# Kernel tuning notes

Hardware: AMD Instinct MI355X
Metric: run time of the kernel (lower is better)

The kernel has to match this reference:

```python
import jax, jax.numpy as jnp
import numpy as np

B, T, DIN = 1024, 256, 128
UNITS, OUT = 512, 64
INTER, CMD, MOTOR = 269, 179, 64  # AutoNCP(512, 64) layer split
SENS_FANOUT, INTER_FANOUT, MOTOR_FANIN = 134, 89, 89
LAYER_DIMS = [(DIN, INTER), (INTER, CMD), (CMD, MOTOR)]


def _layer_mask(rng, n_in, n_h, fanout=None, fanin=None):
    # sparse prev-layer -> layer block, dense recurrent block (ncps WiredCfCCell)
    m = np.zeros((n_in, n_h), dtype=bool)
    if fanout is not None:
        for i in range(n_in):
            m[i, rng.choice(n_h, size=fanout, replace=False)] = True
    else:
        for j in range(n_h):
            m[rng.choice(n_in, size=fanin, replace=False), j] = True
    full = np.concatenate([m, np.ones((n_h, n_h), dtype=bool)], axis=0)
    return jnp.asarray(full.T)  # (n_h, n_in + n_h): Linear weight layout


def setup_inputs() -> dict:
    key = jax.random.key(0)
    ks = jax.random.split(key, 30)
    rng = np.random.RandomState(22222)
    d = {}
    d["x"] = jax.random.normal(ks[0], (B, T, DIN), dtype=jnp.float32)
    d["hidden"] = jnp.zeros((B, UNITS), dtype=jnp.float32)
    d["mask0"] = _layer_mask(rng, DIN, INTER, fanout=SENS_FANOUT)
    d["mask1"] = _layer_mask(rng, INTER, CMD, fanout=INTER_FANOUT)
    d["mask2"] = _layer_mask(rng, CMD, MOTOR, fanin=MOTOR_FANIN)
    ki = 1
    for li, (n_in, n_h) in enumerate(LAYER_DIMS):
        cat = n_in + n_h
        s = 1.0 / float(np.sqrt(cat))
        for nm in ("ff1", "ff2", "ta", "tb"):
            d[f"{nm}_w{li}"] = jax.random.uniform(ks[ki], (n_h, cat), minval=-s, maxval=s, dtype=jnp.float32); ki += 1
            d[f"{nm}_b{li}"] = jax.random.uniform(ks[ki], (n_h,), minval=-s, maxval=s, dtype=jnp.float32); ki += 1
    sf = 1.0 / float(np.sqrt(MOTOR))
    d["fc_w"] = jax.random.uniform(ks[ki], (OUT, MOTOR), minval=-sf, maxval=sf, dtype=jnp.float32)
    d["fc_b"] = jax.random.uniform(ks[ki + 1], (OUT,), minval=-sf, maxval=sf, dtype=jnp.float32)
    return d


def _cfc_cell(inp, h, w1, b1, w2, b2, wa, ba, wb, bb):
    xc = jnp.concatenate([inp, h], axis=-1)
    ff1 = jnp.tanh(xc @ w1.T + b1)
    ff2 = jnp.tanh(xc @ w2.T + b2)
    ts = 1.0  # default elapsed time in CfC when no timespans given
    t_interp = jax.nn.sigmoid((xc @ wa.T + ba) * ts + (xc @ wb.T + bb))
    return ff1 * (1.0 - t_interp) + t_interp * ff2


def reference(x, hidden, mask0, mask1, mask2,
              ff1_w0, ff1_b0, ff2_w0, ff2_b0, ta_w0, ta_b0, tb_w0, tb_b0,
              ff1_w1, ff1_b1, ff2_w1, ff2_b1, ta_w1, ta_b1, tb_w1, tb_b1,
              ff1_w2, ff1_b2, ff2_w2, ff2_b2, ta_w2, ta_b2, tb_w2, tb_b2,
              fc_w, fc_b):
    m0 = mask0.astype(ff1_w0.dtype)
    m1 = mask1.astype(ff1_w1.dtype)
    m2 = mask2.astype(ff1_w2.dtype)
    layers = (
        (ff1_w0 * m0, ff1_b0, ff2_w0 * m0, ff2_b0, ta_w0, ta_b0, tb_w0, tb_b0),
        (ff1_w1 * m1, ff1_b1, ff2_w1 * m1, ff2_b1, ta_w1, ta_b1, tb_w1, tb_b1),
        (ff1_w2 * m2, ff1_b2, ff2_w2 * m2, ff2_b2, ta_w2, ta_b2, tb_w2, tb_b2),
    )
    h0 = hidden[:, :INTER]
    h1 = hidden[:, INTER:INTER + CMD]
    h2 = hidden[:, INTER + CMD:]

    def step(carry, xt):
        c0, c1, c2 = carry
        n0 = _cfc_cell(xt, c0, *layers[0])  # inter layer
        n1 = _cfc_cell(n0, c1, *layers[1])  # command layer
        n2 = _cfc_cell(n1, c2, *layers[2])  # motor layer
        return (n0, n1, n2), n2

    (f0, f1, f2), outs = jax.lax.scan(step, (h0, h1, h2), jnp.swapaxes(x, 0, 1))
    predictions = jnp.einsum('tbm,om->bto', outs, fc_w) + fc_b  # (B,T,OUT)
    hn = jnp.concatenate([f0, f1, f2], axis=-1)  # (B,UNITS)
    return predictions, hn
```

## Files before the change

kernel.cpp:

```cpp
#include <hip/hip_runtime.h>
#include <math.h>


namespace {
constexpr int kBatch = 1024;
constexpr int kT     = 256;
constexpr int kDIN   = 128;
constexpr int kUNITS = 512;
constexpr int kINTER = 269;
constexpr int kCMD   = 179;
constexpr int kMOTOR = 64;
constexpr int kOUT   = 64;

constexpr int kCAT0 = kDIN + kINTER;
constexpr int kCAT1 = kINTER + kCMD;
constexpr int kCAT2 = kCMD + kMOTOR;

constexpr int kC0r = 3 * kINTER;
constexpr int kC1r = 3 * kCMD;
constexpr int kC2r = 3 * kMOTOR;
constexpr int kC0p = 808;
constexpr int kC1p = 538;
constexpr int kC2p = 192;
constexpr int kP0 = 404;
constexpr int kP1 = 269;
constexpr int kP2 = 96;
constexpr int kK40 = 100;
constexpr int kK41 = 112;
constexpr int kK42 = 64;
constexpr int kS0 = kK40 * 4;
constexpr int kS1 = kK41 * 4;
constexpr int kS2 = kK42 * 4;

constexpr int kQ0 = kK40 * kC0p;
constexpr int kQ1 = kK41 * kC1p;
constexpr int kQ2 = kK42 * kC2p;
constexpr int kQ  = kQ0 + kQ1 + kQ2;
constexpr int kBCN = kC0p + kC1p + kC2p;
constexpr int kBCOff = kQ * 4;

constexpr int kMT = 4;
constexpr int kNT = 1024;

static_assert(kK40 % 4 == 0 && kK41 % 4 == 0 && kK42 % 4 == 0, "ping-pong");
}

__device__ __forceinline__ int detect_mask_mode(const void* m0) {
  const unsigned int* w = (const unsigned int*)m0;
  if (w[32] == 0x01010101u && w[33] == 0x01010101u &&
      w[34] == 0x01010101u && w[35] == 0x01010101u)
    return 0;
  if (w[128] == 0x3F800000u && w[129] == 0x3F800000u && w[130] == 0x3F800000u)
    return 2;
  return 1;
}

__device__ __forceinline__ bool mask_at(const void* mk, int idx, int mode) {
  if (mode == 0) return ((const unsigned char*)mk)[idx] != 0;
  if (mode == 1) return ((const int*)mk)[idx] != 0;
  return ((const float*)mk)[idx] != 0.0f;
}

__global__ void prep_kernel(
    const void* __restrict__ m0_, const void* __restrict__ m1_,
    const void* __restrict__ m2_,
    const float* __restrict__ f1w0, const float* __restrict__ f2w0,
    const float* __restrict__ taw0, const float* __restrict__ tbw0,
    const float* __restrict__ f1w1, const float* __restrict__ f2w1,
    const float* __restrict__ taw1, const float* __restrict__ tbw1,
    const float* __restrict__ f1w2, const float* __restrict__ f2w2,
    const float* __restrict__ taw2, const float* __restrict__ tbw2,
    const float* __restrict__ f1b0, const float* __restrict__ f2b0,
    const float* __restrict__ tab0, const float* __restrict__ tbb0,
    const float* __restrict__ f1b1, const float* __restrict__ f2b1,
    const float* __restrict__ tab1, const float* __restrict__ tbb1,
    const float* __restrict__ f1b2, const float* __restrict__ f2b2,
    const float* __restrict__ tab2, const float* __restrict__ tbb2,
    float* __restrict__ ws) {
  int i = blockIdx.x * 256 + threadIdx.x;
  const int mode = detect_mask_mode(m0_);
  if (i < kQ) {
    int qi, NCp, ncols, cat, nh, baseq;
    const void* mk;
    const float *wf1, *wf2, *wta, *wtb;
    if (i < kQ0) {
      qi = i; NCp = kC0p; ncols = kC0r; cat = kCAT0; nh = kINTER; mk = m0_;
      wf1 = f1w0; wf2 = f2w0; wta = taw0; wtb = tbw0; baseq = 0;
    } else if (i < kQ0 + kQ1) {
      qi = i - kQ0; NCp = kC1p; ncols = kC1r; cat = kCAT1; nh = kCMD; mk = m1_;
      wf1 = f1w1; wf2 = f2w1; wta = taw1; wtb = tbw1; baseq = kQ0;
    } else {
      qi = i - kQ0 - kQ1; NCp = kC2p; ncols = kC2r; cat = kCAT2; nh = kMOTOR;
      mk = m2_;
      wf1 = f1w2; wf2 = f2w2; wta = taw2; wtb = tbw2; baseq = kQ0 + kQ1;
    }
    int k4 = qi / NCp;
    int j  = qi % NCp;
    float v[4] = {0.0f, 0.0f, 0.0f, 0.0f};
    if (j < ncols) {
#pragma unroll
      for (int kk = 0; kk < 4; ++kk) {
        int k = k4 * 4 + kk;
        float r = 0.0f;
        if (k < cat) {
          if (j < nh) {
            r = mask_at(mk, j * cat + k, mode) ? wf1[j * cat + k] : 0.0f;
          } else if (j < 2 * nh) {
            int jj = j - nh;
            r = mask_at(mk, jj * cat + k, mode) ? wf2[jj * cat + k] : 0.0f;
          } else {
            int jj = j - 2 * nh;
            r = wta[jj * cat + k] + wtb[jj * cat + k];
          }
        }
        v[kk] = r;
      }
    }
    ((float4*)ws)[baseq + qi] = make_float4(v[0], v[1], v[2], v[3]);
  } else if (i < kQ + kBCN) {
    int pos = i - kQ;
    int j = pos;
    int nh, ncols;
    const float *bf1, *bf2, *bta, *btb;
    if (j < kC0p) {
      nh = kINTER; ncols = kC0r;
      bf1 = f1b0; bf2 = f2b0; bta = tab0; btb = tbb0;
    } else if (j < kC0p + kC1p) {
      j -= kC0p; nh = kCMD; ncols = kC1r;
      bf1 = f1b1; bf2 = f2b1; bta = tab1; btb = tbb1;
    } else {
      j -= kC0p + kC1p; nh = kMOTOR; ncols = kC2r;
      bf1 = f1b2; bf2 = f2b2; bta = tab2; btb = tbb2;
    }
    float r = 0.0f;
    if (j < ncols) {
      if (j < nh) r = bf1[j];
      else if (j < 2 * nh) r = bf2[j - nh];
      else r = bta[j - 2 * nh] + btb[j - 2 * nh];
    }
    ws[kBCOff + pos] = r;
  }
}

template <int AST>
__device__ __forceinline__ void fma_blk(const float4 wA, const float4 wB,
                                        const float* __restrict__ ak,
                                        float (&aA)[kMT], float (&aB)[kMT]) {
#pragma unroll
  for (int r = 0; r < kMT; ++r) {
    float4 av = *(const float4*)(ak + r * AST);
    aA[r] = fmaf(wA.x, av.x, aA[r]);
    aA[r] = fmaf(wA.y, av.y, aA[r]);
    aA[r] = fmaf(wA.z, av.z, aA[r]);
    aA[r] = fmaf(wA.w, av.w, aA[r]);
    aB[r] = fmaf(wB.x, av.x, aB[r]);
    aB[r] = fmaf(wB.y, av.y, aB[r]);
    aB[r] = fmaf(wB.z, av.z, aB[r]);
    aB[r] = fmaf(wB.w, av.w, aB[r]);
  }
}

template <int NK4, int NCOLS, int AST, int PST>
__device__ __forceinline__ void mv2(const float4* __restrict__ wp,
                                    const float* __restrict__ a,
                                    float* __restrict__ pc,
                                    const float* __restrict__ bias,
                                    int jA, int jB) {
  float aA[kMT], aB[kMT];
  const float bA = bias[jA], bB = bias[jB];
#pragma unroll
  for (int r = 0; r < kMT; ++r) { aA[r] = bA; aB[r] = bB; }
  const float4* pA = wp + jA;
  const float4* pB = wp + jB;
  float4 wA0 = pA[0 * NCOLS], wB0 = pB[0 * NCOLS];
  float4 wA1 = pA[1 * NCOLS], wB1 = pB[1 * NCOLS];
  float4 vA0 = pA[2 * NCOLS], vB0 = pB[2 * NCOLS];
  float4 vA1 = pA[3 * NCOLS], vB1 = pB[3 * NCOLS];
  const float* ak = a;
  int k4 = 0;
#pragma unroll 1
  for (; k4 + 8 <= NK4; k4 += 4) {
    fma_blk<AST>(wA0, wB0, ak, aA, aB);
    fma_blk<AST>(wA1, wB1, ak + 4, aA, aB);
    wA0 = pA[(k4 + 4) * NCOLS]; wB0 = pB[(k4 + 4) * NCOLS];
    wA1 = pA[(k4 + 5) * NCOLS]; wB1 = pB[(k4 + 5) * NCOLS];
    fma_blk<AST>(vA0, vB0, ak + 8, aA, aB);
    fma_blk<AST>(vA1, vB1, ak + 12, aA, aB);
    vA0 = pA[(k4 + 6) * NCOLS]; vB0 = pB[(k4 + 6) * NCOLS];
    vA1 = pA[(k4 + 7) * NCOLS]; vB1 = pB[(k4 + 7) * NCOLS];
    ak += 16;
  }
  fma_blk<AST>(wA0, wB0, ak, aA, aB);
  fma_blk<AST>(wA1, wB1, ak + 4, aA, aB);
  fma_blk<AST>(vA0, vB0, ak + 8, aA, aB);
  fma_blk<AST>(vA1, vB1, ak + 12, aA, aB);
#pragma unroll
  for (int r = 0; r < kMT; ++r) {
    pc[r * PST + jA] = aA[r];
    pc[r * PST + jB] = aB[r];
  }
}

__device__ __forceinline__ float cfc_combine(float p1, float p2, float pt) {
  float f1 = tanhf(p1);
  float f2 = tanhf(p2);
  float ti = 1.0f / (1.0f + expf(-pt));
  return f1 + ti * (f2 - f1);
}

__global__ __launch_bounds__(kNT) void ncp_main(
    const float* __restrict__ x, const float* __restrict__ hidden,
    const float* __restrict__ ws, const float* __restrict__ fcw,
    const float* __restrict__ fcb, float* __restrict__ out) {
  __shared__ __align__(16) float xc0[kMT][kS0];
  __shared__ __align__(16) float xc1[kMT][kS1];
  __shared__ __align__(16) float xc2[kMT][kS2];
  __shared__ __align__(16) float pa0[kMT][kC0p];
  __shared__ __align__(16) float pa1[kMT][kC1p];
  __shared__ __align__(16) float pa2[kMT][kC2p];
  __shared__ float s_fcwT[64 * 64];
  __shared__ float s_bc[kBCN];
  __shared__ float s_fcb[64];

  const int tid = threadIdx.x;
  const int b0 = blockIdx.x * kMT;

#pragma unroll
  for (int r = 0; r < kMT; ++r) {
    if (tid < kS0) xc0[r][tid] = 0.0f;
    if (tid < kS1) xc1[r][tid] = 0.0f;
    if (tid < kS2) xc2[r][tid] = 0.0f;
  }
  __syncthreads();
  for (int i = tid; i < kMT * kUNITS; i += kNT) {
    int r = i >> 9, u = i & 511;
    float v = hidden[(size_t)(b0 + r) * kUNITS + u];
    if (u < kINTER) xc0[r][kDIN + u] = v;
    else if (u < kINTER + kCMD) xc1[r][u] = v;
    else xc2[r][kCMD + (u - (kINTER + kCMD))] = v;
  }
  for (int i = tid; i < kBCN; i += kNT) s_bc[i] = ws[kBCOff + i];
  if (tid < 64) s_fcb[tid] = fcb[tid];
  for (int i = tid; i < 64 * 64; i += kNT) {
    int m = i >> 6, o = i & 63;
    s_fcwT[i] = fcw[o * 64 + m];
  }
  if (tid < 128) {
    int r = tid >> 5, d4 = tid & 31;
    *(float4*)&xc0[r][d4 * 4] =
        *(const float4*)&x[(size_t)(b0 + r) * (kT * kDIN) + d4 * 4];
  }
  __syncthreads();

  const float4* wp0 = (const float4*)ws;
  const float4* wp1 = wp0 + kQ0;
  const float4* wp2 = wp1 + kQ1;

  for (int p = 0; p < kT + 3; ++p) {
    if (tid < 448) {
      if (p < kT && tid < kP0)
        mv2<kK40, kC0p, kS0, kC0p>(wp0, &xc0[0][0], &pa0[0][0], s_bc,
                                   tid, tid + kP0);
    } else if (tid < 768) {
      const int pi = tid - 448;
      if (p >= 1 && p <= kT && pi < kP1)
        mv2<kK41, kC1p, kS1, kC1p>(wp1, &xc1[0][0], &pa1[0][0], s_bc + kC0p,
                                   pi, pi + kP1);
    } else if (tid < 896) {
      const int pi = tid - 768;
      if (p >= 2 && p <= kT + 1 && pi < kP2)
        mv2<kK42, kC2p, kS2, kC2p>(wp2, &xc2[0][0], &pa2[0][0],
                                   s_bc + kC0p + kC1p, pi, pi + kP2);
    } else if (p >= 3) {
      const int i2 = tid - 896;
      const int o = i2 & 63;
      const int rb = (i2 >> 6) << 1;
      const int t_fc = p - 3;
      float a0 = s_fcb[o], a1 = s_fcb[o];
      for (int m = 0; m < kMOTOR; ++m) {
        float w = s_fcwT[m * 64 + o];
        a0 = fmaf(xc2[rb][kCMD + m], w, a0);
        a1 = fmaf(xc2[rb + 1][kCMD + m], w, a1);
      }
      size_t base = (size_t)(b0 + rb) * (kT * kOUT) + (size_t)t_fc * kOUT + o;
      out[base] = a0;
      out[base + (size_t)kT * kOUT] = a1;
    }
    __syncthreads();
    if (tid < kINTER) {
      if (p < kT) {
#pragma unroll
        for (int r = 0; r < kMT; ++r) {
          float v = cfc_combine(pa0[r][tid], pa0[r][tid + kINTER],
                                pa0[r][tid + 2 * kINTER]);
          xc1[r][tid] = v;
          xc0[r][kDIN + tid] = v;
        }
      }
    } else if (tid >= 448 && tid < 448 + kCMD) {
      if (p >= 1 && p <= kT) {
        const int j = tid - 448;
#pragma unroll
        for (int r = 0; r < kMT; ++r) {
          float v = cfc_combine(pa1[r][j], pa1[r][j + kCMD],
                                pa1[r][j + 2 * kCMD]);
          xc2[r][j] = v;
          xc1[r][kINTER + j] = v;
        }
      }
    } else if (tid >= 768 && tid < 768 + kMOTOR) {
      if (p >= 2 && p <= kT + 1) {
        const int j = tid - 768;
#pragma unroll
        for (int r = 0; r < kMT; ++r) {
          float v = cfc_combine(pa2[r][j], pa2[r][j + kMOTOR],
                                pa2[r][j + 2 * kMOTOR]);
          xc2[r][kCMD + j] = v;
        }
      }
    } else if (tid >= 896) {
      if (p + 1 < kT) {
        const int i2 = tid - 896;
        const int r = i2 >> 5, d4 = i2 & 31;
        *(float4*)&xc0[r][d4 * 4] =
            *(const float4*)&x[(size_t)(b0 + r) * (kT * kDIN) +
                               (size_t)(p + 1) * kDIN + d4 * 4];
      }
    }
    __syncthreads();
  }

  const size_t hnoff = (size_t)kBatch * kT * kOUT;
  for (int i = tid; i < kMT * kUNITS; i += kNT) {
    int r = i >> 9, u = i & 511;
    float v;
    if (u < kINTER) v = xc0[r][kDIN + u];
    else if (u < kINTER + kCMD) v = xc1[r][u];
    else v = xc2[r][kCMD + (u - (kINTER + kCMD))];
    out[hnoff + (size_t)(b0 + r) * kUNITS + u] = v;
  }
}

extern "C" void kernel_launch(void* const* d_in, const int* in_sizes, int n_in,
                              void* d_out, int out_size, void* d_ws, size_t ws_size,
                              hipStream_t stream) {
  (void)in_sizes; (void)n_in; (void)out_size; (void)ws_size;
  const float* x = (const float*)d_in[0];
  const float* hidden = (const float*)d_in[1];
  const void* m0 = d_in[2];
  const void* m1 = d_in[3];
  const void* m2 = d_in[4];
  const float* f1w0 = (const float*)d_in[5];
  const float* f1b0 = (const float*)d_in[6];
  const float* f2w0 = (const float*)d_in[7];
  const float* f2b0 = (const float*)d_in[8];
  const float* taw0 = (const float*)d_in[9];
  const float* tab0 = (const float*)d_in[10];
  const float* tbw0 = (const float*)d_in[11];
  const float* tbb0 = (const float*)d_in[12];
  const float* f1w1 = (const float*)d_in[13];
  const float* f1b1 = (const float*)d_in[14];
  const float* f2w1 = (const float*)d_in[15];
  const float* f2b1 = (const float*)d_in[16];
  const float* taw1 = (const float*)d_in[17];
  const float* tab1 = (const float*)d_in[18];
  const float* tbw1 = (const float*)d_in[19];
  const float* tbb1 = (const float*)d_in[20];
  const float* f1w2 = (const float*)d_in[21];
  const float* f1b2 = (const float*)d_in[22];
  const float* f2w2 = (const float*)d_in[23];
  const float* f2b2 = (const float*)d_in[24];
  const float* taw2 = (const float*)d_in[25];
  const float* tab2 = (const float*)d_in[26];
  const float* tbw2 = (const float*)d_in[27];
  const float* tbb2 = (const float*)d_in[28];
  const float* fcw = (const float*)d_in[29];
  const float* fcb = (const float*)d_in[30];
  float* ws = (float*)d_ws;
  float* out = (float*)d_out;

  const int prep_items = kQ + kBCN;
  prep_kernel<<<(prep_items + 255) / 256, 256, 0, stream>>>(
      m0, m1, m2,
      f1w0, f2w0, taw0, tbw0,
      f1w1, f2w1, taw1, tbw1,
      f1w2, f2w2, taw2, tbw2,
      f1b0, f2b0, tab0, tbb0,
      f1b1, f2b1, tab1, tbb1,
      f1b2, f2b2, tab2, tbb2,
      ws);

  ncp_main<<<kBatch / kMT, kNT, 0, stream>>>(x, hidden, ws, fcw, fcb, out);
}
```

Measured before the change: 8.694 ms.

## Compute four adjacent output columns per thread and shrink block to 768 threads

Each matvec thread now computes four adjacent output columns instead of two strided ones. Each shared-memory activation read feeds four columns, and results go out as float4 stores. The block drops from 1024 to 768 threads, with the role ranges (layer matvecs, combine, x prefetch, FC output) remapped. The FC output stage now uses 64 threads that each handle four rows. The goal is less LDS traffic per FMA and less per-step barrier cost. The cost is more registers per thread (16 accumulators plus 16 float4 weight registers) and fewer threads to hide latency.

```diff
diff --git a/kernel.cpp b/kernel.cpp
--- a/kernel.cpp
+++ b/kernel.cpp
@@ -20,11 +20,11 @@
 constexpr int kC1r = 3 * kCMD;
 constexpr int kC2r = 3 * kMOTOR;
 constexpr int kC0p = 808;
-constexpr int kC1p = 538;
+constexpr int kC1p = 540;
 constexpr int kC2p = 192;
-constexpr int kP0 = 404;
-constexpr int kP1 = 269;
-constexpr int kP2 = 96;
+constexpr int kP0 = 202;
+constexpr int kP1 = 135;
+constexpr int kP2 = 48;
 constexpr int kK40 = 100;
 constexpr int kK41 = 112;
 constexpr int kK42 = 64;
@@ -40,9 +40,10 @@
 constexpr int kBCOff = kQ * 4;
 
 constexpr int kMT = 4;
-constexpr int kNT = 1024;
+constexpr int kNT = 768;
 
 static_assert(kK40 % 4 == 0 && kK41 % 4 == 0 && kK42 % 4 == 0, "ping-pong");
+static_assert(kC0p % 4 == 0 && kC1p % 4 == 0 && kC2p % 4 == 0, "4-col");
 }
 
 __device__ __forceinline__ int detect_mask_mode(const void* m0) {
@@ -143,61 +144,71 @@
 }
 
 template <int AST>
-__device__ __forceinline__ void fma_blk(const float4 wA, const float4 wB,
-                                        const float* __restrict__ ak,
-                                        float (&aA)[kMT], float (&aB)[kMT]) {
+__device__ __forceinline__ void fma4(const float4 (&w)[4],
+                                     const float* __restrict__ ak,
+                                     float (&acc)[4][kMT]) {
 #pragma unroll
   for (int r = 0; r < kMT; ++r) {
     float4 av = *(const float4*)(ak + r * AST);
-    aA[r] = fmaf(wA.x, av.x, aA[r]);
-    aA[r] = fmaf(wA.y, av.y, aA[r]);
-    aA[r] = fmaf(wA.z, av.z, aA[r]);
-    aA[r] = fmaf(wA.w, av.w, aA[r]);
-    aB[r] = fmaf(wB.x, av.x, aB[r]);
-    aB[r] = fmaf(wB.y, av.y, aB[r]);
-    aB[r] = fmaf(wB.z, av.z, aB[r]);
-    aB[r] = fmaf(wB.w, av.w, aB[r]);
+#pragma unroll
+    for (int c = 0; c < 4; ++c) {
+      acc[c][r] = fmaf(w[c].x, av.x, acc[c][r]);
+      acc[c][r] = fmaf(w[c].y, av.y, acc[c][r]);
+      acc[c][r] = fmaf(w[c].z, av.z, acc[c][r]);
+      acc[c][r] = fmaf(w[c].w, av.w, acc[c][r]);
+    }
   }
 }
 
 template <int NK4, int NCOLS, int AST, int PST>
-__device__ __forceinline__ void mv2(const float4* __restrict__ wp,
+__device__ __forceinline__ void mv4(const float4* __restrict__ wp,
                                     const float* __restrict__ a,
                                     float* __restrict__ pc,
                                     const float* __restrict__ bias,
-                                    int jA, int jB) {
-  float aA[kMT], aB[kMT];
-  const float bA = bias[jA], bB = bias[jB];
-#pragma unroll
-  for (int r = 0; r < kMT; ++r) { aA[r] = bA; aB[r] = bB; }
-  const float4* pA = wp + jA;
-  const float4* pB = wp + jB;
-  float4 wA0 = pA[0 * NCOLS], wB0 = pB[0 * NCOLS];
-  float4 wA1 = pA[1 * NCOLS], wB1 = pB[1 * NCOLS];
-  float4 vA0 = pA[2 * NCOLS], vB0 = pB[2 * NCOLS];
-  float4 vA1 = pA[3 * NCOLS], vB1 = pB[3 * NCOLS];
+                                    int jq) {
+  const float4* pw = wp + 4 * jq;
+  float acc[4][kMT];
+#pragma unroll
+  for (int c = 0; c < 4; ++c) {
+    const float b = bias[4 * jq + c];
+#pragma unroll
+    for (int r = 0; r < kMT; ++r) acc[c][r] = b;
+  }
+  float4 U0[4], U1[4], V0[4], V1[4];
+#pragma unroll
+  for (int c = 0; c < 4; ++c) {
+    U0[c] = pw[0 * NCOLS + c];
+    U1[c] = pw[1 * NCOLS + c];
+    V0[c] = pw[2 * NCOLS + c];
+    V1[c] = pw[3 * NCOLS + c];
+  }
   const float* ak = a;
-  int k4 = 0;
 #pragma unroll 1
-  for (; k4 + 8 <= NK4; k4 += 4) {
-    fma_blk<AST>(wA0, wB0, ak, aA, aB);
-    fma_blk<AST>(wA1, wB1, ak + 4, aA, aB);
-    wA0 = pA[(k4 + 4) * NCOLS]; wB0 = pB[(k4 + 4) * NCOLS];
-    wA1 = pA[(k4 + 5) * NCOLS]; wB1 = pB[(k4 + 5) * NCOLS];
-    fma_blk<AST>(vA0, vB0, ak + 8, aA, aB);
-    fma_blk<AST>(vA1, vB1, ak + 12, aA, aB);
-    vA0 = pA[(k4 + 6) * NCOLS]; vB0 = pB[(k4 + 6) * NCOLS];
-    vA1 = pA[(k4 + 7) * NCOLS]; vB1 = pB[(k4 + 7) * NCOLS];
+  for (int k4 = 0; k4 + 8 <= NK4; k4 += 4) {
+    fma4<AST>(U0, ak, acc);
+    fma4<AST>(U1, ak + 4, acc);
+#pragma unroll
+    for (int c = 0; c < 4; ++c) {
+      U0[c] = pw[(k4 + 4) * NCOLS + c];
+      U1[c] = pw[(k4 + 5) * NCOLS + c];
+    }
+    fma4<AST>(V0, ak + 8, acc);
+    fma4<AST>(V1, ak + 12, acc);
+#pragma unroll
+    for (int c = 0; c < 4; ++c) {
+      V0[c] = pw[(k4 + 6) * NCOLS + c];
+      V1[c] = pw[(k4 + 7) * NCOLS + c];
+    }
     ak += 16;
   }
-  fma_blk<AST>(wA0, wB0, ak, aA, aB);
-  fma_blk<AST>(wA1, wB1, ak + 4, aA, aB);
-  fma_blk<AST>(vA0, vB0, ak + 8, aA, aB);
-  fma_blk<AST>(vA1, vB1, ak + 12, aA, aB);
+  fma4<AST>(U0, ak, acc);
+  fma4<AST>(U1, ak + 4, acc);
+  fma4<AST>(V0, ak + 8, acc);
+  fma4<AST>(V1, ak + 12, acc);
 #pragma unroll
   for (int r = 0; r < kMT; ++r) {
-    pc[r * PST + jA] = aA[r];
-    pc[r * PST + jB] = aB[r];
+    float4 o = make_float4(acc[0][r], acc[1][r], acc[2][r], acc[3][r]);
+    *(float4*)&pc[r * PST + 4 * jq] = o;
   }
 }
 
@@ -257,34 +268,39 @@
   const float4* wp2 = wp1 + kQ1;
 
   for (int p = 0; p < kT + 3; ++p) {
-    if (tid < 448) {
+    if (tid < 256) {
       if (p < kT && tid < kP0)
-        mv2<kK40, kC0p, kS0, kC0p>(wp0, &xc0[0][0], &pa0[0][0], s_bc,
-                                   tid, tid + kP0);
-    } else if (tid < 768) {
+        mv4<kK40, kC0p, kS0, kC0p>(wp0, &xc0[0][0], &pa0[0][0], s_bc, tid);
+    } else if (tid < 448) {
+      const int pi = tid - 256;
+      if (p >= 1 && p <= kT && pi < kP1)
+        mv4<kK41, kC1p, kS1, kC1p>(wp1, &xc1[0][0], &pa1[0][0], s_bc + kC0p,
+                                   pi);
+    } else if (tid < 512) {
       const int pi = tid - 448;
-      if (p >= 1 && p <= kT && pi < kP1)
-        mv2<kK41, kC1p, kS1, kC1p>(wp1, &xc1[0][0], &pa1[0][0], s_bc + kC0p,
-                                   pi, pi + kP1);
-    } else if (tid < 896) {
-      const int pi = tid - 768;
       if (p >= 2 && p <= kT + 1 && pi < kP2)
-        mv2<kK42, kC2p, kS2, kC2p>(wp2, &xc2[0][0], &pa2[0][0],
-                                   s_bc + kC0p + kC1p, pi, pi + kP2);
-    } else if (p >= 3) {
-      const int i2 = tid - 896;
-      const int o = i2 & 63;
-      const int rb = (i2 >> 6) << 1;
-      const int t_fc = p - 3;
-      float a0 = s_fcb[o], a1 = s_fcb[o];
-      for (int m = 0; m < kMOTOR; ++m) {
-        float w = s_fcwT[m * 64 + o];
-        a0 = fmaf(xc2[rb][kCMD + m], w, a0);
-        a1 = fmaf(xc2[rb + 1][kCMD + m], w, a1);
-      }
-      size_t base = (size_t)(b0 + rb) * (kT * kOUT) + (size_t)t_fc * kOUT + o;
-      out[base] = a0;
-      out[base + (size_t)kT * kOUT] = a1;
+        mv4<kK42, kC2p, kS2, kC2p>(wp2, &xc2[0][0], &pa2[0][0],
+                                   s_bc + kC0p + kC1p, pi);
+    } else if (tid >= 704) {
+      if (p >= 3) {
+        const int o = tid - 704;
+        const int t_fc = p - 3;
+        float a0 = s_fcb[o], a1 = a0, a2 = a0, a3 = a0;
+        for (int m = 0; m < kMOTOR; ++m) {
+          float w = s_fcwT[m * 64 + o];
+          a0 = fmaf(xc2[0][kCMD + m], w, a0);
+          a1 = fmaf(xc2[1][kCMD + m], w, a1);
+          a2 = fmaf(xc2[2][kCMD + m], w, a2);
+          a3 = fmaf(xc2[3][kCMD + m], w, a3);
+        }
+        size_t base =
+            (size_t)b0 * (kT * kOUT) + (size_t)t_fc * kOUT + o;
+        const size_t rstride = (size_t)kT * kOUT;
+        out[base] = a0;
+        out[base + rstride] = a1;
+        out[base + 2 * rstride] = a2;
+        out[base + 3 * rstride] = a3;
+      }
     }
     __syncthreads();
     if (tid < kINTER) {
@@ -297,9 +313,9 @@
           xc0[r][kDIN + tid] = v;
         }
       }
-    } else if (tid >= 448 && tid < 448 + kCMD) {
+    } else if (tid >= 320 && tid < 320 + kCMD) {
       if (p >= 1 && p <= kT) {
-        const int j = tid - 448;
+        const int j = tid - 320;
 #pragma unroll
         for (int r = 0; r < kMT; ++r) {
           float v = cfc_combine(pa1[r][j], pa1[r][j + kCMD],
@@ -308,9 +324,9 @@
           xc1[r][kINTER + j] = v;
         }
       }
-    } else if (tid >= 768 && tid < 768 + kMOTOR) {
+    } else if (tid >= 512 && tid < 512 + kMOTOR) {
       if (p >= 2 && p <= kT + 1) {
-        const int j = tid - 768;
+        const int j = tid - 512;
 #pragma unroll
         for (int r = 0; r < kMT; ++r) {
           float v = cfc_combine(pa2[r][j], pa2[r][j + kMOTOR],
@@ -318,9 +334,9 @@
           xc2[r][kCMD + j] = v;
         }
       }
-    } else if (tid >= 896) {
+    } else if (tid >= 576 && tid < 704) {
       if (p + 1 < kT) {
-        const int i2 = tid - 896;
+        const int i2 = tid - 576;
         const int r = i2 >> 5, d4 = i2 & 31;
         *(float4*)&xc0[r][d4 * 4] =
             *(const float4*)&x[(size_t)(b0 + r) * (kT * kDIN) +
```

After: 11.02 ms. 1.27x slower.
